# Kernel tuning notes

Measured on AMD Instinct MI355X. Metric: run time of the kernel, lower is better.

The kernel has to match this reference:

```python
import jax, jax.numpy as jnp
import numpy as np

EPS = 1e-8  # torch nn.CosineSimilarity default eps


def setup_inputs() -> dict:
    key = jax.random.key(0)
    k1, k2, k3 = jax.random.split(key, 3)
    N, K, Q, CH, H, W, D = 32, 5, 15, 3, 84, 84, 1600
    supp_x = jax.random.normal(k1, (N, K, CH, H, W), dtype=jnp.float32)
    query_x = jax.random.normal(k2, (N, Q, CH, H, W), dtype=jnp.float32)
    W_enc = jax.random.normal(k3, (CH * H * W, D), dtype=jnp.float32) * 0.02
    return {"supp_x": supp_x, "query_x": query_x, "W_enc": W_enc}


def reference(supp_x, query_x, W_enc):
    N, K = supp_x.shape[0], supp_x.shape[1]
    Q = query_x.shape[1]
    # encoder: flatten image -> linear projection (stands in for backbone)
    s_feat = supp_x.reshape(N * K, -1) @ W_enc          # (N*K, D)
    x_proto = s_feat.reshape(N, K, -1).mean(axis=1)     # (N, D) class prototypes
    x_q = query_x.reshape(N * Q, -1) @ W_enc            # (N*Q, D)
    # cosine similarity: L2-normalize with eps clamp, then single matmul
    qn = x_q / jnp.maximum(jnp.linalg.norm(x_q, axis=1, keepdims=True), EPS)
    pn = x_proto / jnp.maximum(jnp.linalg.norm(x_proto, axis=1, keepdims=True), EPS)
    sim = qn @ pn.T                                     # (N*Q, N)
    return jax.nn.log_softmax(sim, axis=1)
```

## Files before the change

### kernel.cpp

```cpp
#include <hip/hip_runtime.h>
#include <hip/hip_bf16.h>
#include <cstdint>
#include <cstddef>

namespace {

constexpr int NCLS   = 32;
constexpr int KSHOT  = 5;
constexpr int FDIM   = 21168;
constexpr int KPAD   = 21248;
constexpr int DDIM   = 1600;
constexpr int NROW   = 512;
constexpr int NQROW  = 480;
constexpr int NKT    = 332;
constexpr int MAXS   = 18;

using short8 = __attribute__((ext_vector_type(8))) short;
using f32x4  = __attribute__((ext_vector_type(4))) float;

__device__ __forceinline__ unsigned short f2bf(float x) {
    union { float f; unsigned u; } v; v.f = x;
    unsigned r = v.u + 0x7fffu + ((v.u >> 16) & 1u);
    return (unsigned short)(r >> 16);
}

__device__ __forceinline__ unsigned short f2bfc(float x) {
    __hip_bfloat16 h = __float2bfloat16(x);
    unsigned short u;
    __builtin_memcpy(&u, &h, 2);
    return u;
}

__global__ void prep_A(const float* __restrict__ supp,
                       const float* __restrict__ query,
                       unsigned short* __restrict__ A) {
    const int r = blockIdx.y;
    const int u = blockIdx.x * blockDim.x + threadIdx.x;
    if (u >= KPAD / 4) return;
    const int c = u * 4;
    float4 v = make_float4(0.f, 0.f, 0.f, 0.f);
    if (c < FDIM) {
        if (r < NCLS) {
            const float* s = supp + (size_t)r * KSHOT * FDIM + c;
            float4 a0 = *(const float4*)(s);
            float4 a1 = *(const float4*)(s + FDIM);
            float4 a2 = *(const float4*)(s + 2 * FDIM);
            float4 a3 = *(const float4*)(s + 3 * FDIM);
            float4 a4 = *(const float4*)(s + 4 * FDIM);
            v.x = (a0.x + a1.x + a2.x + a3.x + a4.x) * 0.2f;
            v.y = (a0.y + a1.y + a2.y + a3.y + a4.y) * 0.2f;
            v.z = (a0.z + a1.z + a2.z + a3.z + a4.z) * 0.2f;
            v.w = (a0.w + a1.w + a2.w + a3.w + a4.w) * 0.2f;
        } else {
            v = *(const float4*)(query + (size_t)(r - NCLS) * FDIM + c);
        }
    }
    ushort4 o;
    o.x = f2bf(v.x); o.y = f2bf(v.y); o.z = f2bf(v.z); o.w = f2bf(v.w);
    *(ushort4*)(A + (size_t)r * KPAD + c) = o;
}

__global__ __launch_bounds__(512, 2) void gemm13(
        const unsigned short* __restrict__ A,
        const float* __restrict__ W,
        float* __restrict__ Cpart, int S) {
    __shared__ unsigned short Al[2][256 * 64];
    __shared__ unsigned short Bl[2][256 * 64];

    const int nwg = gridDim.x, orig = blockIdx.x;
    const int xcd = orig & 7, q8 = nwg >> 3, r8 = nwg & 7;
    const int wgid = (xcd < r8 ? xcd * (q8 + 1) : r8 * (q8 + 1) + (xcd - r8) * q8)
                   + (orig >> 3);

    const int s   = wgid / 14;
    const int rem = wgid % 14;
    const int mt  = rem & 1;
    const int nt  = rem >> 1;
    const int m0  = mt * 256;
    const int n0  = nt * 256;
    const int t0  = (NKT * s) / S;
    const int t1  = (NKT * (s + 1)) / S;
    const int tmax = t1 - 1;

    const int tid  = threadIdx.x;
    const int lane = tid & 63;
    const int w    = tid >> 6;
    const int wr   = w & 1;
    const int wc   = w >> 1;
    const int g    = lane >> 4;
    const int r15  = lane & 15;

    const int srow = lane >> 3, sblk = lane & 7;
    const unsigned short* Asrc[4];
    int AdstOff[4];
    #pragma unroll
    for (int i = 0; i < 4; ++i) {
        const int r = w * 32 + i * 8 + srow;
        Asrc[i] = A + (size_t)(m0 + r) * KPAD + (size_t)((sblk ^ (r & 7)) * 8);
        AdstOff[i] = (w * 32 + i * 8) * 64;
    }

    const int nq = tid & 63;
    const int kh = tid >> 6;
    const int ncb = min(n0 + 4 * nq, DDIM - 4);
    const float* Wp = W + ncb;
    const int bq = (kh ^ (nq & 7)) * 8;

    f32x4 acc[8][4];
    #pragma unroll
    for (int i = 0; i < 8; ++i)
        #pragma unroll
        for (int j = 0; j < 4; ++j)
            acc[i][j] = (f32x4){0.f, 0.f, 0.f, 0.f};

    float4 wv[8];

#define LOAD_W(t) { const int kb_ = (t) * 64 + kh * 8; _Pragma("unroll") \
    for (int i = 0; i < 8; ++i) { \
        const int k_ = kb_ + i; \
        wv[i] = (k_ < FDIM) ? *(const float4*)(Wp + (size_t)k_ * DDIM) \
                            : make_float4(0.f, 0.f, 0.f, 0.f); } }

#define PACK_B(buf) { \
    { uint4 P; \
      P.x = f2bfc(wv[0].x) | ((unsigned)f2bfc(wv[1].x) << 16); \
      P.y = f2bfc(wv[2].x) | ((unsigned)f2bfc(wv[3].x) << 16); \
      P.z = f2bfc(wv[4].x) | ((unsigned)f2bfc(wv[5].x) << 16); \
      P.w = f2bfc(wv[6].x) | ((unsigned)f2bfc(wv[7].x) << 16); \
      *(uint4*)&Bl[buf][(4 * nq + 0) * 64 + bq] = P; } \
    { uint4 P; \
      P.x = f2bfc(wv[0].y) | ((unsigned)f2bfc(wv[1].y) << 16); \
      P.y = f2bfc(wv[2].y) | ((unsigned)f2bfc(wv[3].y) << 16); \
      P.z = f2bfc(wv[4].y) | ((unsigned)f2bfc(wv[5].y) << 16); \
      P.w = f2bfc(wv[6].y) | ((unsigned)f2bfc(wv[7].y) << 16); \
      *(uint4*)&Bl[buf][(4 * nq + 1) * 64 + bq] = P; } \
    { uint4 P; \
      P.x = f2bfc(wv[0].z) | ((unsigned)f2bfc(wv[1].z) << 16); \
      P.y = f2bfc(wv[2].z) | ((unsigned)f2bfc(wv[3].z) << 16); \
      P.z = f2bfc(wv[4].z) | ((unsigned)f2bfc(wv[5].z) << 16); \
      P.w = f2bfc(wv[6].z) | ((unsigned)f2bfc(wv[7].z) << 16); \
      *(uint4*)&Bl[buf][(4 * nq + 2) * 64 + bq] = P; } \
    { uint4 P; \
      P.x = f2bfc(wv[0].w) | ((unsigned)f2bfc(wv[1].w) << 16); \
      P.y = f2bfc(wv[2].w) | ((unsigned)f2bfc(wv[3].w) << 16); \
      P.z = f2bfc(wv[4].w) | ((unsigned)f2bfc(wv[5].w) << 16); \
      P.w = f2bfc(wv[6].w) | ((unsigned)f2bfc(wv[7].w) << 16); \
      *(uint4*)&Bl[buf][(4 * nq + 3) * 64 + bq] = P; } }

#define GLDS_A(buf, t) { _Pragma("unroll") \
    for (int i = 0; i < 4; ++i) \
        __builtin_amdgcn_global_load_lds( \
            (const __attribute__((address_space(1))) void*)(Asrc[i] + (size_t)(t) * 64), \
            (__attribute__((address_space(3))) void*)(&Al[buf][AdstOff[i]]), 16, 0, 0); }

#define COMPUTE(buf) { _Pragma("unroll") \
    for (int kk = 0; kk < 2; ++kk) { \
        const int q_ = kk * 4 + g; \
        short8 bf_[4]; \
        _Pragma("unroll") \
        for (int ns = 0; ns < 4; ++ns) { \
            const int n_ = wc * 64 + ns * 16 + r15; \
            bf_[ns] = *(const short8*)&Bl[buf][n_ * 64 + ((q_ ^ ((n_ >> 2) & 7)) * 8)]; \
        } \
        _Pragma("unroll") \
        for (int ms = 0; ms < 8; ++ms) { \
            const int R_ = wr * 128 + ms * 16 + r15; \
            short8 af_ = *(const short8*)&Al[buf][R_ * 64 + ((q_ ^ (R_ & 7)) * 8)]; \
            _Pragma("unroll") \
            for (int ns = 0; ns < 4; ++ns) \
                acc[ms][ns] = __builtin_amdgcn_mfma_f32_16x16x32_bf16( \
                    af_, bf_[ns], acc[ms][ns], 0, 0, 0); } } }

    LOAD_W(t0);
    PACK_B(0);
    GLDS_A(0, t0);
    LOAD_W(min(t0 + 1, tmax));
    __syncthreads();

    int cur = 0;
    for (int t = t0; t < t1; ++t) {
        const bool m1 = (t + 1 < t1);
        if (m1) {
            PACK_B(cur ^ 1);
            LOAD_W(min(t + 2, tmax));
            GLDS_A(cur ^ 1, t + 1);
        }
        COMPUTE(cur);
        __syncthreads();
        if (m1) cur ^= 1;
    }

#undef LOAD_W
#undef PACK_B
#undef GLDS_A
#undef COMPUTE

    float* Cp = Cpart + (size_t)s * NROW * DDIM;
    #pragma unroll
    for (int ms = 0; ms < 8; ++ms) {
        const int row = m0 + wr * 128 + ms * 16 + g * 4;
        #pragma unroll
        for (int ns = 0; ns < 4; ++ns) {
            const int col = n0 + wc * 64 + ns * 16 + r15;
            if (col < DDIM) {
                #pragma unroll
                for (int r = 0; r < 4; ++r)
                    Cp[(size_t)(row + r) * DDIM + col] = acc[ms][ns][r];
            }
        }
    }
}

__global__ void reduce_norm(const float* __restrict__ Cpart,
                            float* __restrict__ C,
                            float* __restrict__ inv_norm, int S) {
    const int row = blockIdx.x;
    const int tid = threadIdx.x;
    float acc = 0.f;
    for (int c4 = tid * 4; c4 < DDIM; c4 += 1024) {
        float4 v = make_float4(0.f, 0.f, 0.f, 0.f);
        for (int s2 = 0; s2 < S; ++s2) {
            float4 p = *(const float4*)&Cpart[((size_t)s2 * NROW + row) * DDIM + c4];
            v.x += p.x; v.y += p.y; v.z += p.z; v.w += p.w;
        }
        *(float4*)&C[(size_t)row * DDIM + c4] = v;
        acc += v.x * v.x + v.y * v.y + v.z * v.z + v.w * v.w;
    }
    __shared__ float red[4];
    #pragma unroll
    for (int off = 32; off > 0; off >>= 1) acc += __shfl_xor(acc, off);
    if ((tid & 63) == 0) red[tid >> 6] = acc;
    __syncthreads();
    if (tid == 0) {
        float a = red[0] + red[1] + red[2] + red[3];
        inv_norm[row] = 1.f / fmaxf(sqrtf(a), 1e-8f);
    }
}

__global__ void simlog(const float* __restrict__ C,
                       const float* __restrict__ inv_norm,
                       float* __restrict__ out) {
    __shared__ float qs[DDIM];
    __shared__ float sims[NCLS];
    const int r = blockIdx.x;
    const int tid = threadIdx.x;
    const float* qrow = C + (size_t)(NCLS + r) * DDIM;
    for (int c = tid; c < DDIM; c += 256) qs[c] = qrow[c];
    __syncthreads();
    const float invq = inv_norm[NCLS + r];
    const int lane = tid & 63, w = tid >> 6;
    #pragma unroll
    for (int j = 0; j < 8; ++j) {
        const int p = w * 8 + j;
        const float* prow = C + (size_t)p * DDIM;
        float d = 0.f;
        for (int c = lane; c < DDIM; c += 64) d += qs[c] * prow[c];
        #pragma unroll
        for (int off = 32; off > 0; off >>= 1) d += __shfl_xor(d, off);
        if (lane == 0) sims[p] = d * invq * inv_norm[p];
    }
    __syncthreads();
    if (w == 0) {
        float v = (lane < NCLS) ? sims[lane] : -1e30f;
        float m = v;
        #pragma unroll
        for (int off = 32; off > 0; off >>= 1) m = fmaxf(m, __shfl_xor(m, off));
        float e = (lane < NCLS) ? expf(v - m) : 0.f;
        float ss = e;
        #pragma unroll
        for (int off = 32; off > 0; off >>= 1) ss += __shfl_xor(ss, off);
        if (lane < NCLS) out[(size_t)r * NCLS + lane] = v - m - logf(ss);
    }
}

}


extern "C" void kernel_launch(void* const* d_in, const int* in_sizes, int n_in,
                              void* d_out, int out_size, void* d_ws, size_t ws_size,
                              hipStream_t stream) {
    const float* supp  = (const float*)d_in[0];
    const float* query = (const float*)d_in[1];
    const float* Wenc  = (const float*)d_in[2];
    float* out = (float*)d_out;

    const size_t fixedA = 21757952;
    const size_t slot   = (size_t)NROW * DDIM * 4;

    int S = MAXS;
    if (ws_size > fixedA + slot + 4096) {
        size_t avail = (ws_size - fixedA - slot - 4096) / slot;
        if ((size_t)S > avail) S = (int)avail;
    }
    if (S < 1) S = 1;

    char* ws = (char*)d_ws;
    unsigned short* A = (unsigned short*)ws;
    float* Cpart    = (float*)(ws + fixedA);
    float* C        = (float*)(ws + fixedA + (size_t)S * slot);
    float* inv_norm = (float*)(ws + fixedA + (size_t)(S + 1) * slot);

    hipLaunchKernelGGL(prep_A, dim3((KPAD / 4 + 255) / 256, NROW), dim3(256),
                       0, stream, supp, query, A);
    hipLaunchKernelGGL(gemm13, dim3(14 * S), dim3(512), 0, stream,
                       A, Wenc, Cpart, S);
    hipLaunchKernelGGL(reduce_norm, dim3(NROW), dim3(256), 0, stream,
                       Cpart, C, inv_norm, S);
    hipLaunchKernelGGL(simlog, dim3(NQROW), dim3(256), 0, stream,
                       C, inv_norm, out);
}
```

Before: 157.2 us.

## Double GEMM workgroup to 1024 threads and store split-K partials as bf16

The GEMM workgroup grows from 8 to 16 waves over the same 256x256 tile, so each wave holds a 64x64 accumulator tile instead of 128x64. Each thread now loads and packs half as many W rows, and the B-tile swizzle is reworked for 8-byte writes. The goal is more latency hiding per CU and less register pressure. Split-K partial results are now written as bf16 rather than fp32, halving the partial-sum traffic between the GEMM and the reduction kernel, at the cost of extra rounding error in each partial.

After: 140.2 us. 1.12x faster.

```diff
diff --git a/kernel.cpp b/kernel.cpp
--- a/kernel.cpp
+++ b/kernel.cpp
@@ -29,6 +29,11 @@
     unsigned short u;
     __builtin_memcpy(&u, &h, 2);
     return u;
+}
+
+__device__ __forceinline__ float bf2f(unsigned short u) {
+    union { unsigned u; float f; } v; v.u = (unsigned)u << 16;
+    return v.f;
 }
 
 __global__ void prep_A(const float* __restrict__ supp,
@@ -60,10 +65,10 @@
     *(ushort4*)(A + (size_t)r * KPAD + c) = o;
 }
 
-__global__ __launch_bounds__(512, 2) void gemm13(
+__global__ __launch_bounds__(1024, 4) void gemm14(
         const unsigned short* __restrict__ A,
         const float* __restrict__ W,
-        float* __restrict__ Cpart, int S) {
+        unsigned short* __restrict__ Cpart, int S) {
     __shared__ unsigned short Al[2][256 * 64];
     __shared__ unsigned short Bl[2][256 * 64];
 
@@ -85,70 +90,63 @@
     const int tid  = threadIdx.x;
     const int lane = tid & 63;
     const int w    = tid >> 6;
-    const int wr   = w & 1;
-    const int wc   = w >> 1;
+    const int wr   = w & 3;
+    const int wc   = w >> 2;
     const int g    = lane >> 4;
     const int r15  = lane & 15;
 
     const int srow = lane >> 3, sblk = lane & 7;
-    const unsigned short* Asrc[4];
-    int AdstOff[4];
-    #pragma unroll
-    for (int i = 0; i < 4; ++i) {
-        const int r = w * 32 + i * 8 + srow;
+    const unsigned short* Asrc[2];
+    int AdstOff[2];
+    #pragma unroll
+    for (int i = 0; i < 2; ++i) {
+        const int r = w * 16 + i * 8 + srow;
         Asrc[i] = A + (size_t)(m0 + r) * KPAD + (size_t)((sblk ^ (r & 7)) * 8);
-        AdstOff[i] = (w * 32 + i * 8) * 64;
+        AdstOff[i] = (w * 16 + i * 8) * 64;
     }
 
     const int nq = tid & 63;
     const int kh = tid >> 6;
     const int ncb = min(n0 + 4 * nq, DDIM - 4);
     const float* Wp = W + ncb;
-    const int bq = (kh ^ (nq & 7)) * 8;
-
-    f32x4 acc[8][4];
-    #pragma unroll
-    for (int i = 0; i < 8; ++i)
+    const int ysw = (nq & 7) * 2;
+    const int slot = kh ^ ysw;
+
+    f32x4 acc[4][4];
+    #pragma unroll
+    for (int i = 0; i < 4; ++i)
         #pragma unroll
         for (int j = 0; j < 4; ++j)
             acc[i][j] = (f32x4){0.f, 0.f, 0.f, 0.f};
 
-    float4 wv[8];
-
-#define LOAD_W(t) { const int kb_ = (t) * 64 + kh * 8; _Pragma("unroll") \
-    for (int i = 0; i < 8; ++i) { \
+    float4 wv[4];
+
+#define LOAD_W(t) { const int kb_ = (t) * 64 + kh * 4; _Pragma("unroll") \
+    for (int i = 0; i < 4; ++i) { \
         const int k_ = kb_ + i; \
         wv[i] = (k_ < FDIM) ? *(const float4*)(Wp + (size_t)k_ * DDIM) \
                             : make_float4(0.f, 0.f, 0.f, 0.f); } }
 
 #define PACK_B(buf) { \
-    { uint4 P; \
+    { uint2 P; \
       P.x = f2bfc(wv[0].x) | ((unsigned)f2bfc(wv[1].x) << 16); \
       P.y = f2bfc(wv[2].x) | ((unsigned)f2bfc(wv[3].x) << 16); \
-      P.z = f2bfc(wv[4].x) | ((unsigned)f2bfc(wv[5].x) << 16); \
-      P.w = f2bfc(wv[6].x) | ((unsigned)f2bfc(wv[7].x) << 16); \
-      *(uint4*)&Bl[buf][(4 * nq + 0) * 64 + bq] = P; } \
-    { uint4 P; \
+      *(uint2*)&Bl[buf][(4 * nq + 0) * 64 + slot * 4] = P; } \
+    { uint2 P; \
       P.x = f2bfc(wv[0].y) | ((unsigned)f2bfc(wv[1].y) << 16); \
       P.y = f2bfc(wv[2].y) | ((unsigned)f2bfc(wv[3].y) << 16); \
-      P.z = f2bfc(wv[4].y) | ((unsigned)f2bfc(wv[5].y) << 16); \
-      P.w = f2bfc(wv[6].y) | ((unsigned)f2bfc(wv[7].y) << 16); \
-      *(uint4*)&Bl[buf][(4 * nq + 1) * 64 + bq] = P; } \
-    { uint4 P; \
+      *(uint2*)&Bl[buf][(4 * nq + 1) * 64 + slot * 4] = P; } \
+    { uint2 P; \
       P.x = f2bfc(wv[0].z) | ((unsigned)f2bfc(wv[1].z) << 16); \
       P.y = f2bfc(wv[2].z) | ((unsigned)f2bfc(wv[3].z) << 16); \
-      P.z = f2bfc(wv[4].z) | ((unsigned)f2bfc(wv[5].z) << 16); \
-      P.w = f2bfc(wv[6].z) | ((unsigned)f2bfc(wv[7].z) << 16); \
-      *(uint4*)&Bl[buf][(4 * nq + 2) * 64 + bq] = P; } \
-    { uint4 P; \
+      *(uint2*)&Bl[buf][(4 * nq + 2) * 64 + slot * 4] = P; } \
+    { uint2 P; \
       P.x = f2bfc(wv[0].w) | ((unsigned)f2bfc(wv[1].w) << 16); \
       P.y = f2bfc(wv[2].w) | ((unsigned)f2bfc(wv[3].w) << 16); \
-      P.z = f2bfc(wv[4].w) | ((unsigned)f2bfc(wv[5].w) << 16); \
-      P.w = f2bfc(wv[6].w) | ((unsigned)f2bfc(wv[7].w) << 16); \
-      *(uint4*)&Bl[buf][(4 * nq + 3) * 64 + bq] = P; } }
+      *(uint2*)&Bl[buf][(4 * nq + 3) * 64 + slot * 4] = P; } }
 
 #define GLDS_A(buf, t) { _Pragma("unroll") \
-    for (int i = 0; i < 4; ++i) \
+    for (int i = 0; i < 2; ++i) \
         __builtin_amdgcn_global_load_lds( \
             (const __attribute__((address_space(1))) void*)(Asrc[i] + (size_t)(t) * 64), \
             (__attribute__((address_space(3))) void*)(&Al[buf][AdstOff[i]]), 16, 0, 0); }
@@ -160,11 +158,12 @@
         _Pragma("unroll") \
         for (int ns = 0; ns < 4; ++ns) { \
             const int n_ = wc * 64 + ns * 16 + r15; \
-            bf_[ns] = *(const short8*)&Bl[buf][n_ * 64 + ((q_ ^ ((n_ >> 2) & 7)) * 8)]; \
+            const int p_ = (2 * q_) ^ (((n_ >> 2) & 7) * 2); \
+            bf_[ns] = *(const short8*)&Bl[buf][n_ * 64 + p_ * 4]; \
         } \
         _Pragma("unroll") \
-        for (int ms = 0; ms < 8; ++ms) { \
-            const int R_ = wr * 128 + ms * 16 + r15; \
+        for (int ms = 0; ms < 4; ++ms) { \
+            const int R_ = wr * 64 + ms * 16 + r15; \
             short8 af_ = *(const short8*)&Al[buf][R_ * 64 + ((q_ ^ (R_ & 7)) * 8)]; \
             _Pragma("unroll") \
             for (int ns = 0; ns < 4; ++ns) \
@@ -173,8 +172,8 @@
 
     LOAD_W(t0);
     PACK_B(0);
+    LOAD_W(min(t0 + 1, tmax));
     GLDS_A(0, t0);
-    LOAD_W(min(t0 + 1, tmax));
     __syncthreads();
 
     int cur = 0;
@@ -195,23 +194,23 @@
 #undef GLDS_A
 #undef COMPUTE
 
-    float* Cp = Cpart + (size_t)s * NROW * DDIM;
-    #pragma unroll
-    for (int ms = 0; ms < 8; ++ms) {
-        const int row = m0 + wr * 128 + ms * 16 + g * 4;
+    unsigned short* Cp = Cpart + (size_t)s * NROW * DDIM;
+    #pragma unroll
+    for (int ms = 0; ms < 4; ++ms) {
+        const int row = m0 + wr * 64 + ms * 16 + g * 4;
         #pragma unroll
         for (int ns = 0; ns < 4; ++ns) {
             const int col = n0 + wc * 64 + ns * 16 + r15;
             if (col < DDIM) {
                 #pragma unroll
                 for (int r = 0; r < 4; ++r)
-                    Cp[(size_t)(row + r) * DDIM + col] = acc[ms][ns][r];
+                    Cp[(size_t)(row + r) * DDIM + col] = f2bfc(acc[ms][ns][r]);
             }
         }
     }
 }
 
-__global__ void reduce_norm(const float* __restrict__ Cpart,
+__global__ void reduce_norm(const unsigned short* __restrict__ Cpart,
                             float* __restrict__ C,
                             float* __restrict__ inv_norm, int S) {
     const int row = blockIdx.x;
@@ -220,8 +219,9 @@
     for (int c4 = tid * 4; c4 < DDIM; c4 += 1024) {
         float4 v = make_float4(0.f, 0.f, 0.f, 0.f);
         for (int s2 = 0; s2 < S; ++s2) {
-            float4 p = *(const float4*)&Cpart[((size_t)s2 * NROW + row) * DDIM + c4];
-            v.x += p.x; v.y += p.y; v.z += p.z; v.w += p.w;
+            ushort4 u = *(const ushort4*)&Cpart[((size_t)s2 * NROW + row) * DDIM + c4];
+            v.x += bf2f(u.x); v.y += bf2f(u.y);
+            v.z += bf2f(u.z); v.w += bf2f(u.w);
         }
         *(float4*)&C[(size_t)row * DDIM + c4] = v;
         acc += v.x * v.x + v.y * v.y + v.z * v.z + v.w * v.w;
@@ -285,24 +285,25 @@
     float* out = (float*)d_out;
 
     const size_t fixedA = 21757952;
-    const size_t slot   = (size_t)NROW * DDIM * 4;
+    const size_t slotBf = (size_t)NROW * DDIM * 2;
+    const size_t slotC  = (size_t)NROW * DDIM * 4;
 
     int S = MAXS;
-    if (ws_size > fixedA + slot + 4096) {
-        size_t avail = (ws_size - fixedA - slot - 4096) / slot;
+    if (ws_size > fixedA + slotC + 4096) {
+        size_t avail = (ws_size - fixedA - slotC - 4096) / slotBf;
         if ((size_t)S > avail) S = (int)avail;
     }
     if (S < 1) S = 1;
 
     char* ws = (char*)d_ws;
     unsigned short* A = (unsigned short*)ws;
-    float* Cpart    = (float*)(ws + fixedA);
-    float* C        = (float*)(ws + fixedA + (size_t)S * slot);
-    float* inv_norm = (float*)(ws + fixedA + (size_t)(S + 1) * slot);
+    unsigned short* Cpart = (unsigned short*)(ws + fixedA);
+    float* C        = (float*)(ws + fixedA + (size_t)S * slotBf);
+    float* inv_norm = (float*)(ws + fixedA + (size_t)S * slotBf + slotC);
 
     hipLaunchKernelGGL(prep_A, dim3((KPAD / 4 + 255) / 256, NROW), dim3(256),
                        0, stream, supp, query, A);
-    hipLaunchKernelGGL(gemm13, dim3(14 * S), dim3(512), 0, stream,
+    hipLaunchKernelGGL(gemm14, dim3(14 * S), dim3(1024), 0, stream,
                        A, Wenc, Cpart, S);
     hipLaunchKernelGGL(reduce_norm, dim3(NROW), dim3(256), 0, stream,
                        Cpart, C, inv_norm, S);
```

## Split GEMM k-step into four barrier-synchronized MFMA phases with interleaved loads; store bf16 partials

Applied to the files above, without the earlier changes.

The GEMM main loop becomes four phases. Each phase loads its A/B fragments, waits at a raw s_barrier, and runs its MFMAs at raised priority. B packing, A global-to-LDS loads and W prefetch are interleaved between phases with explicit waitcnt control in place of __syncthreads. The warp layout and the A/B staging swizzle are reorganised, and W loads clamp the index instead of branching. Split-K partials are stored as bf16 rather than fp32 to halve partial traffic, which adds rounding error to the accumulated result.

New measurement: 158.3 us. About the same (+0.7%).

```diff
diff --git a/kernel.cpp b/kernel.cpp
--- a/kernel.cpp
+++ b/kernel.cpp
@@ -29,6 +29,11 @@
     unsigned short u;
     __builtin_memcpy(&u, &h, 2);
     return u;
+}
+
+__device__ __forceinline__ float bf2f(unsigned short u) {
+    union { unsigned u; float f; } v; v.u = (unsigned)u << 16;
+    return v.f;
 }
 
 __global__ void prep_A(const float* __restrict__ supp,
@@ -60,12 +65,12 @@
     *(ushort4*)(A + (size_t)r * KPAD + c) = o;
 }
 
-__global__ __launch_bounds__(512, 2) void gemm13(
+__global__ __launch_bounds__(512, 2) void gemm16(
         const unsigned short* __restrict__ A,
         const float* __restrict__ W,
-        float* __restrict__ Cpart, int S) {
-    __shared__ unsigned short Al[2][256 * 64];
-    __shared__ unsigned short Bl[2][256 * 64];
+        unsigned short* __restrict__ Cpart, int S) {
+    __shared__ unsigned short Abuf[2][256 * 64];
+    __shared__ unsigned short Bbuf[2][256 * 64];
 
     const int nwg = gridDim.x, orig = blockIdx.x;
     const int xcd = orig & 7, q8 = nwg >> 3, r8 = nwg & 7;
@@ -85,26 +90,24 @@
     const int tid  = threadIdx.x;
     const int lane = tid & 63;
     const int w    = tid >> 6;
-    const int wr   = w & 1;
-    const int wc   = w >> 1;
-    const int g    = lane >> 4;
+    const int wr   = w >> 2;
+    const int wc   = w & 3;
+    const int gl   = lane >> 4;
     const int r15  = lane & 15;
 
-    const int srow = lane >> 3, sblk = lane & 7;
+    const int asw = ((lane & 7) ^ (lane >> 3)) * 8;
     const unsigned short* Asrc[4];
     int AdstOff[4];
     #pragma unroll
     for (int i = 0; i < 4; ++i) {
-        const int r = w * 32 + i * 8 + srow;
-        Asrc[i] = A + (size_t)(m0 + r) * KPAD + (size_t)((sblk ^ (r & 7)) * 8);
-        AdstOff[i] = (w * 32 + i * 8) * 64;
-    }
-
-    const int nq = tid & 63;
-    const int kh = tid >> 6;
-    const int ncb = min(n0 + 4 * nq, DDIM - 4);
+        const int r = i * 64 + w * 8 + (lane >> 3);
+        Asrc[i] = A + (size_t)(m0 + r) * KPAD + asw;
+        AdstOff[i] = (i * 64 + w * 8) * 64;
+    }
+
+    const int ncb = min(n0 + 4 * lane, DDIM - 4);
     const float* Wp = W + ncb;
-    const int bq = (kh ^ (nq & 7)) * 8;
+    const int gsw = (w ^ (lane & 7)) * 8;
 
     f32x4 acc[8][4];
     #pragma unroll
@@ -115,103 +118,131 @@
 
     float4 wv[8];
 
-#define LOAD_W(t) { const int kb_ = (t) * 64 + kh * 8; _Pragma("unroll") \
+#define FENCE() asm volatile("" ::: "memory")
+
+#define LOAD_W(t) { _Pragma("unroll") \
     for (int i = 0; i < 8; ++i) { \
-        const int k_ = kb_ + i; \
-        wv[i] = (k_ < FDIM) ? *(const float4*)(Wp + (size_t)k_ * DDIM) \
-                            : make_float4(0.f, 0.f, 0.f, 0.f); } }
-
-#define PACK_B(buf) { \
+        const int k_ = (t) * 64 + w * 8 + i; \
+        const int kc_ = min(k_, FDIM - 1);    \
+        wv[i] = *(const float4*)(Wp + (size_t)kc_ * DDIM); } }
+
+#define PACK01(buf) { \
     { uint4 P; \
       P.x = f2bfc(wv[0].x) | ((unsigned)f2bfc(wv[1].x) << 16); \
       P.y = f2bfc(wv[2].x) | ((unsigned)f2bfc(wv[3].x) << 16); \
       P.z = f2bfc(wv[4].x) | ((unsigned)f2bfc(wv[5].x) << 16); \
       P.w = f2bfc(wv[6].x) | ((unsigned)f2bfc(wv[7].x) << 16); \
-      *(uint4*)&Bl[buf][(4 * nq + 0) * 64 + bq] = P; } \
+      *(uint4*)&Bbuf[buf][(4 * lane + 0) * 64 + gsw] = P; } \
     { uint4 P; \
       P.x = f2bfc(wv[0].y) | ((unsigned)f2bfc(wv[1].y) << 16); \
       P.y = f2bfc(wv[2].y) | ((unsigned)f2bfc(wv[3].y) << 16); \
       P.z = f2bfc(wv[4].y) | ((unsigned)f2bfc(wv[5].y) << 16); \
       P.w = f2bfc(wv[6].y) | ((unsigned)f2bfc(wv[7].y) << 16); \
-      *(uint4*)&Bl[buf][(4 * nq + 1) * 64 + bq] = P; } \
+      *(uint4*)&Bbuf[buf][(4 * lane + 1) * 64 + gsw] = P; } }
+
+#define PACK23(buf) { \
     { uint4 P; \
       P.x = f2bfc(wv[0].z) | ((unsigned)f2bfc(wv[1].z) << 16); \
       P.y = f2bfc(wv[2].z) | ((unsigned)f2bfc(wv[3].z) << 16); \
       P.z = f2bfc(wv[4].z) | ((unsigned)f2bfc(wv[5].z) << 16); \
       P.w = f2bfc(wv[6].z) | ((unsigned)f2bfc(wv[7].z) << 16); \
-      *(uint4*)&Bl[buf][(4 * nq + 2) * 64 + bq] = P; } \
+      *(uint4*)&Bbuf[buf][(4 * lane + 2) * 64 + gsw] = P; } \
     { uint4 P; \
       P.x = f2bfc(wv[0].w) | ((unsigned)f2bfc(wv[1].w) << 16); \
       P.y = f2bfc(wv[2].w) | ((unsigned)f2bfc(wv[3].w) << 16); \
       P.z = f2bfc(wv[4].w) | ((unsigned)f2bfc(wv[5].w) << 16); \
       P.w = f2bfc(wv[6].w) | ((unsigned)f2bfc(wv[7].w) << 16); \
-      *(uint4*)&Bl[buf][(4 * nq + 3) * 64 + bq] = P; } }
+      *(uint4*)&Bbuf[buf][(4 * lane + 3) * 64 + gsw] = P; } }
 
 #define GLDS_A(buf, t) { _Pragma("unroll") \
     for (int i = 0; i < 4; ++i) \
         __builtin_amdgcn_global_load_lds( \
             (const __attribute__((address_space(1))) void*)(Asrc[i] + (size_t)(t) * 64), \
-            (__attribute__((address_space(3))) void*)(&Al[buf][AdstOff[i]]), 16, 0, 0); }
-
-#define COMPUTE(buf) { _Pragma("unroll") \
+            (__attribute__((address_space(3))) void*)(&Abuf[buf][AdstOff[i]]), 16, 0, 0); }
+
+#define PHASE(buf, P, ENDWAIT) { \
+    short8 af_[2][2], bf_[2][4]; \
+    _Pragma("unroll") \
     for (int kk = 0; kk < 2; ++kk) { \
-        const int q_ = kk * 4 + g; \
-        short8 bf_[4]; \
+        const int q_ = kk * 4 + gl; \
+        _Pragma("unroll") \
+        for (int mi = 0; mi < 2; ++mi) { \
+            const int R_ = wr * 128 + (2 * (P) + mi) * 16 + r15; \
+            af_[kk][mi] = *(const short8*)&Abuf[buf][R_ * 64 + ((q_ ^ (R_ & 7)) * 8)]; \
+        } \
         _Pragma("unroll") \
         for (int ns = 0; ns < 4; ++ns) { \
             const int n_ = wc * 64 + ns * 16 + r15; \
-            bf_[ns] = *(const short8*)&Bl[buf][n_ * 64 + ((q_ ^ ((n_ >> 2) & 7)) * 8)]; \
+            bf_[kk][ns] = *(const short8*)&Bbuf[buf][n_ * 64 + (((q_ ^ ((n_ >> 2) & 7))) * 8)]; \
         } \
+    } \
+    ENDWAIT; \
+    __builtin_amdgcn_s_barrier(); \
+    __builtin_amdgcn_s_setprio(1); \
+    _Pragma("unroll") \
+    for (int kk = 0; kk < 2; ++kk) \
         _Pragma("unroll") \
-        for (int ms = 0; ms < 8; ++ms) { \
-            const int R_ = wr * 128 + ms * 16 + r15; \
-            short8 af_ = *(const short8*)&Al[buf][R_ * 64 + ((q_ ^ (R_ & 7)) * 8)]; \
+        for (int mi = 0; mi < 2; ++mi) \
             _Pragma("unroll") \
             for (int ns = 0; ns < 4; ++ns) \
-                acc[ms][ns] = __builtin_amdgcn_mfma_f32_16x16x32_bf16( \
-                    af_, bf_[ns], acc[ms][ns], 0, 0, 0); } } }
+                acc[2 * (P) + mi][ns] = __builtin_amdgcn_mfma_f32_16x16x32_bf16( \
+                    af_[kk][mi], bf_[kk][ns], acc[2 * (P) + mi][ns], 0, 0, 0); \
+    __builtin_amdgcn_s_setprio(0); }
+
+#define NOWAIT
+#define TILEWAIT asm volatile("s_waitcnt vmcnt(8) lgkmcnt(0)" ::: "memory")
 
     LOAD_W(t0);
-    PACK_B(0);
+    PACK01(0); PACK23(0);
+    FENCE();
     GLDS_A(0, t0);
+    FENCE();
     LOAD_W(min(t0 + 1, tmax));
-    __syncthreads();
+    TILEWAIT;
+    __builtin_amdgcn_s_barrier();
 
     int cur = 0;
     for (int t = t0; t < t1; ++t) {
-        const bool m1 = (t + 1 < t1);
-        if (m1) {
-            PACK_B(cur ^ 1);
-            LOAD_W(min(t + 2, tmax));
-            GLDS_A(cur ^ 1, t + 1);
-        }
-        COMPUTE(cur);
-        __syncthreads();
-        if (m1) cur ^= 1;
-    }
-
+        PACK01(cur ^ 1);
+        PHASE(cur, 0, NOWAIT);
+        PACK23(cur ^ 1);
+        FENCE();
+        GLDS_A(cur ^ 1, min(t + 1, tmax));
+        PHASE(cur, 1, NOWAIT);
+        FENCE();
+        LOAD_W(min(t + 2, tmax));
+        PHASE(cur, 2, NOWAIT);
+        PHASE(cur, 3, TILEWAIT);
+        cur ^= 1;
+    }
+    asm volatile("s_waitcnt vmcnt(0)" ::: "memory");
+
+#undef FENCE
 #undef LOAD_W
-#undef PACK_B
+#undef PACK01
+#undef PACK23
 #undef GLDS_A
-#undef COMPUTE
-
-    float* Cp = Cpart + (size_t)s * NROW * DDIM;
+#undef PHASE
+#undef NOWAIT
+#undef TILEWAIT
+
+    unsigned short* Cp = Cpart + (size_t)s * NROW * DDIM;
     #pragma unroll
     for (int ms = 0; ms < 8; ++ms) {
-        const int row = m0 + wr * 128 + ms * 16 + g * 4;
+        const int row = m0 + wr * 128 + ms * 16 + gl * 4;
         #pragma unroll
         for (int ns = 0; ns < 4; ++ns) {
             const int col = n0 + wc * 64 + ns * 16 + r15;
             if (col < DDIM) {
                 #pragma unroll
                 for (int r = 0; r < 4; ++r)
-                    Cp[(size_t)(row + r) * DDIM + col] = acc[ms][ns][r];
+                    Cp[(size_t)(row + r) * DDIM + col] = f2bfc(acc[ms][ns][r]);
             }
         }
     }
 }
 
-__global__ void reduce_norm(const float* __restrict__ Cpart,
+__global__ void reduce_norm(const unsigned short* __restrict__ Cpart,
                             float* __restrict__ C,
                             float* __restrict__ inv_norm, int S) {
     const int row = blockIdx.x;
@@ -220,8 +251,9 @@
     for (int c4 = tid * 4; c4 < DDIM; c4 += 1024) {
         float4 v = make_float4(0.f, 0.f, 0.f, 0.f);
         for (int s2 = 0; s2 < S; ++s2) {
-            float4 p = *(const float4*)&Cpart[((size_t)s2 * NROW + row) * DDIM + c4];
-            v.x += p.x; v.y += p.y; v.z += p.z; v.w += p.w;
+            ushort4 u = *(const ushort4*)&Cpart[((size_t)s2 * NROW + row) * DDIM + c4];
+            v.x += bf2f(u.x); v.y += bf2f(u.y);
+            v.z += bf2f(u.z); v.w += bf2f(u.w);
         }
         *(float4*)&C[(size_t)row * DDIM + c4] = v;
         acc += v.x * v.x + v.y * v.y + v.z * v.z + v.w * v.w;
@@ -285,24 +317,25 @@
     float* out = (float*)d_out;
 
     const size_t fixedA = 21757952;
-    const size_t slot   = (size_t)NROW * DDIM * 4;
+    const size_t slotBf = (size_t)NROW * DDIM * 2;
+    const size_t slotC  = (size_t)NROW * DDIM * 4;
 
     int S = MAXS;
-    if (ws_size > fixedA + slot + 4096) {
-        size_t avail = (ws_size - fixedA - slot - 4096) / slot;
+    if (ws_size > fixedA + slotC + 4096) {
+        size_t avail = (ws_size - fixedA - slotC - 4096) / slotBf;
         if ((size_t)S > avail) S = (int)avail;
     }
     if (S < 1) S = 1;
 
     char* ws = (char*)d_ws;
     unsigned short* A = (unsigned short*)ws;
-    float* Cpart    = (float*)(ws + fixedA);
-    float* C        = (float*)(ws + fixedA + (size_t)S * slot);
-    float* inv_norm = (float*)(ws + fixedA + (size_t)(S + 1) * slot);
+    unsigned short* Cpart = (unsigned short*)(ws + fixedA);
+    float* C        = (float*)(ws + fixedA + (size_t)S * slotBf);
+    float* inv_norm = (float*)(ws + fixedA + (size_t)S * slotBf + slotC);
 
     hipLaunchKernelGGL(prep_A, dim3((KPAD / 4 + 255) / 256, NROW), dim3(256),
                        0, stream, supp, query, A);
-    hipLaunchKernelGGL(gemm13, dim3(14 * S), dim3(512), 0, stream,
+    hipLaunchKernelGGL(gemm16, dim3(14 * S), dim3(512), 0, stream,
                        A, Wenc, Cpart, S);
     hipLaunchKernelGGL(reduce_norm, dim3(NROW), dim3(256), 0, stream,
                        Cpart, C, inv_norm, S);
```
